# Kernel optimization log

Measured on AMD Instinct MI355X. Metric: run time of the kernel, lower is better.

Reference implementation:

```python
import jax, jax.numpy as jnp
import numpy as np

D = 1024
H = 16
DH = D // H
RATIO = 4
EPS = 1e-5


def layer_norm(x, g, b):
    mu = jnp.mean(x, axis=-1, keepdims=True)
    var = jnp.mean(jnp.square(x - mu), axis=-1, keepdims=True)
    return (x - mu) * jax.lax.rsqrt(var + EPS) * g + b


def setup_inputs() -> dict:
    key = jax.random.key(0)
    ks = jax.random.split(key, 12)
    s = 1.0 / np.sqrt(D)
    inp = {
        "x": jax.random.normal(ks[0], (4, 2048, D), dtype=jnp.float32),
        "Wq": jax.random.normal(ks[1], (D, D), dtype=jnp.float32) * s,
        "bq": jnp.zeros((D,), jnp.float32),
        "Wk": jax.random.normal(ks[2], (D, D), dtype=jnp.float32) * s,
        "bk": jnp.zeros((D,), jnp.float32),
        "Wv": jax.random.normal(ks[3], (D, D), dtype=jnp.float32) * s,
        "bv": jnp.zeros((D,), jnp.float32),
        "Wfc": jax.random.normal(ks[4], (D, D), dtype=jnp.float32) * s,
        "bfc": jnp.zeros((D,), jnp.float32),
        "ln1_g": jnp.ones((D,), jnp.float32),
        "ln1_b": jnp.zeros((D,), jnp.float32),
        "W1": jax.random.normal(ks[5], (D, D * RATIO), dtype=jnp.float32) * s,
        "b1": jnp.zeros((D * RATIO,), jnp.float32),
        "W2": jax.random.normal(ks[6], (D * RATIO, D), dtype=jnp.float32) * (1.0 / np.sqrt(D * RATIO)),
        "b2": jnp.zeros((D,), jnp.float32),
        "ln2_g": jnp.ones((D,), jnp.float32),
        "ln2_b": jnp.zeros((D,), jnp.float32),
    }
    return inp


def reference(x, Wq, bq, Wk, bk, Wv, bv, Wfc, bfc, ln1_g, ln1_b, W1, b1, W2, b2, ln2_g, ln2_b):
    B, S, _ = x.shape
    # QKV projections -> [B, H, S, DH]
    q = (x @ Wq + bq).reshape(B, S, H, DH).transpose(0, 2, 1, 3)
    k = (x @ Wk + bk).reshape(B, S, H, DH).transpose(0, 2, 1, 3)
    v = (x @ Wv + bv).reshape(B, S, H, DH).transpose(0, 2, 1, 3)
    scores = jnp.einsum("bhqd,bhkd->bhqk", q, k) / np.sqrt(DH)
    w = jax.nn.softmax(scores, axis=-1)
    attn = jnp.einsum("bhqk,bhkd->bhqd", w, v)
    attn = attn.transpose(0, 2, 1, 3).reshape(B, S, D)
    attn_out = attn @ Wfc + bfc  # dropout = identity (droprate=0)
    h = layer_norm(x + attn_out, ln1_g, ln1_b)
    m = jax.nn.relu(h @ W1 + b1)
    m = m @ W2 + b2
    # NOTE: original code applies mlp_norm without residual
    return layer_norm(m, ln2_g, ln2_b)
```

## Files before the change

### kernel.cpp

```cpp
#include <hip/hip_runtime.h>
#include <hip/hip_bf16.h>

#define DEV __device__ __forceinline__

typedef __attribute__((ext_vector_type(8))) short short8;
typedef __attribute__((ext_vector_type(4))) float f32x4;

DEV f32x4 mfma16(short8 a, short8 b, f32x4 c) {
  return __builtin_amdgcn_mfma_f32_16x16x32_bf16(a, b, c, 0, 0, 0);
}

DEV unsigned short f2bf(float f) {
  union { float f; unsigned u; } x; x.f = f;
  unsigned r = x.u + 0x7fffu + ((x.u >> 16) & 1u);
  return (unsigned short)(r >> 16);
}

__global__ __launch_bounds__(256) void cvt_bf16(const float* __restrict__ in,
                                                unsigned short* __restrict__ out,
                                                int n4) {
  int i = blockIdx.x * 256 + threadIdx.x;
  if (i >= n4) return;
  float4 v = ((const float4*)in)[i];
  ushort4 o;
  o.x = f2bf(v.x); o.y = f2bf(v.y); o.z = f2bf(v.z); o.w = f2bf(v.w);
  ((ushort4*)out)[i] = o;
}

__global__ __launch_bounds__(256) void cvtT(const float* __restrict__ W,
                                            unsigned short* __restrict__ Wt,
                                            int K, int N) {
  __shared__ float t[32][33];
  int n0 = blockIdx.x * 32, k0 = blockIdx.y * 32;
  int tx = threadIdx.x, ty = threadIdx.y;
#pragma unroll
  for (int i = 0; i < 4; i++)
    t[ty * 4 + i][tx] = W[(size_t)(k0 + ty * 4 + i) * N + n0 + tx];
  __syncthreads();
#pragma unroll
  for (int i = 0; i < 4; i++)
    Wt[(size_t)(n0 + ty * 4 + i) * K + k0 + tx] = f2bf(t[tx][ty * 4 + i]);
}

enum { M_Q = 0, M_K = 1, M_V = 2, M_RES = 3, M_RELU = 4, M_F32 = 5 };

template <int MODE>
__global__ __launch_bounds__(256, 2)
void gemm_bt(const unsigned short* __restrict__ A,
             const unsigned short* __restrict__ Bt,
             const float* __restrict__ bias,
             const float* __restrict__ res,
             void* __restrict__ outp, int M, int N, int K) {
  __shared__ unsigned short lA[128 * 64];
  __shared__ unsigned short lB[128 * 64];
  const int tid = threadIdx.x;
  const int l = tid & 63, w = tid >> 6;
  const int wr = w >> 1, wc = w & 1;
  const int lr = l & 15, lg = l >> 4;
  const int m0 = blockIdx.x * 128, n0 = blockIdx.y * 128;
  f32x4 acc[4][4] = {};

  for (int k0 = 0; k0 < K; k0 += 64) {
    __syncthreads();
#pragma unroll
    for (int i = 0; i < 4; i++) {
      int off = (i * 256 + tid) * 8;
      int r = off >> 6, c = off & 63;
      __builtin_amdgcn_global_load_lds(
          (const __attribute__((address_space(1))) unsigned int*)(A + (size_t)(m0 + r) * K + k0 + c),
          (__attribute__((address_space(3))) unsigned int*)(lA + off), 16, 0, 0);
    }
#pragma unroll
    for (int i = 0; i < 4; i++) {
      int off = (i * 256 + tid) * 8;
      int r = off >> 6, c = off & 63;
      __builtin_amdgcn_global_load_lds(
          (const __attribute__((address_space(1))) unsigned int*)(Bt + (size_t)(n0 + r) * K + k0 + c),
          (__attribute__((address_space(3))) unsigned int*)(lB + off), 16, 0, 0);
    }
    __syncthreads();
#pragma unroll
    for (int kk = 0; kk < 2; kk++) {
      short8 af[4], bfr[4];
#pragma unroll
      for (int mt = 0; mt < 4; mt++)
        af[mt] = *(const short8*)(lA + (wr * 64 + mt * 16 + lr) * 64 + kk * 32 + lg * 8);
#pragma unroll
      for (int nt = 0; nt < 4; nt++)
        bfr[nt] = *(const short8*)(lB + (wc * 64 + nt * 16 + lr) * 64 + kk * 32 + lg * 8);
#pragma unroll
      for (int mt = 0; mt < 4; mt++)
#pragma unroll
        for (int nt = 0; nt < 4; nt++)
          acc[mt][nt] = mfma16(af[mt], bfr[nt], acc[mt][nt]);
    }
  }

#pragma unroll
  for (int mt = 0; mt < 4; mt++) {
#pragma unroll
    for (int nt = 0; nt < 4; nt++) {
#pragma unroll
      for (int r = 0; r < 4; r++) {
        int row = m0 + wr * 64 + mt * 16 + lg * 4 + r;
        int col = n0 + wc * 64 + nt * 16 + lr;
        float v = acc[mt][nt][r] + bias[col];
        if constexpr (MODE == M_Q || MODE == M_K || MODE == M_V) {
          int b = row >> 11, s = row & 2047;
          int h = col >> 6, dh = col & 63;
          if constexpr (MODE == M_Q) {
            ((unsigned short*)outp)[(((size_t)(b * 16 + h) * 2048 + s) << 6) + dh] = f2bf(v * 0.125f);
          } else if constexpr (MODE == M_K) {
            ((unsigned short*)outp)[(((size_t)(b * 16 + h) * 2048 + s) << 6) + dh] = f2bf(v);
          } else {
            ((unsigned short*)outp)[((size_t)(b * 16 + h) * 64 + dh) * 2048 + s] = f2bf(v);
          }
        } else if constexpr (MODE == M_RES) {
          size_t idx = (size_t)row * N + col;
          ((float*)outp)[idx] = v + res[idx];
        } else if constexpr (MODE == M_RELU) {
          ((unsigned short*)outp)[(size_t)row * N + col] = f2bf(v > 0.f ? v : 0.f);
        } else {
          ((float*)outp)[(size_t)row * N + col] = v;
        }
      }
    }
  }
}

__global__ __launch_bounds__(256, 4)
void flash_attn(const unsigned short* __restrict__ Q,
                const unsigned short* __restrict__ Kb,
                const unsigned short* __restrict__ Vt,
                unsigned short* __restrict__ attnb) {
  const int S = 2048;
  __shared__ unsigned short Qs[64 * 64];
  __shared__ unsigned short Ks[2][64 * 64];
  __shared__ unsigned short Vs[2][64 * 64];
  const int tid = threadIdx.x, l = tid & 63, w = tid >> 6;
  const int lr = l & 15, lg = l >> 4;
  const int bh = blockIdx.y, q0 = blockIdx.x * 64;
  const unsigned short* Qp = Q + (size_t)bh * S * 64;
  const unsigned short* Kp = Kb + (size_t)bh * S * 64;
  const unsigned short* Vp = Vt + (size_t)bh * 64 * S;

  auto stage64 = [&](const unsigned short* gbase, size_t rstride, unsigned short* lds) {
#pragma unroll
    for (int i = 0; i < 2; i++) {
      int off16 = i * 256 + tid;
      int r = off16 >> 3;
      int chs = (off16 & 7) ^ (r & 7);
      __builtin_amdgcn_global_load_lds(
          (const __attribute__((address_space(1))) unsigned int*)(gbase + (size_t)r * rstride + chs * 8),
          (__attribute__((address_space(3))) unsigned int*)(lds + (size_t)off16 * 8), 16, 0, 0);
    }
  };

  stage64(Qp + (size_t)q0 * 64, 64, Qs);
  stage64(Kp, 64, Ks[0]);
  stage64(Vp, S, Vs[0]);
  __syncthreads();

  short8 qf[2];
#pragma unroll
  for (int kk = 0; kk < 2; kk++) {
    int rq = w * 16 + lr;
    qf[kk] = *(const short8*)((char*)Qs + rq * 128 + (((kk * 32 + lg * 8) * 2) ^ ((rq & 7) << 4)));
  }
  unsigned short* Pw = Qs + w * 1024;

  float lpart[4] = {0.f, 0.f, 0.f, 0.f};
  f32x4 oacc[4] = {};

  int cur = 0;
  for (int kv0 = 0; kv0 < S; kv0 += 64) {
    if (kv0 + 64 < S) {
      stage64(Kp + (size_t)(kv0 + 64) * 64, 64, Ks[cur ^ 1]);
      stage64(Vp + (kv0 + 64), S, Vs[cur ^ 1]);
    }
    const unsigned short* Kc = Ks[cur];
    const unsigned short* Vc = Vs[cur];

    f32x4 sa[4] = {};
#pragma unroll
    for (int nt = 0; nt < 4; nt++) {
#pragma unroll
      for (int kk = 0; kk < 2; kk++) {
        int rk = nt * 16 + lr;
        short8 kf = *(const short8*)((const char*)Kc + rk * 128 + (((kk * 32 + lg * 8) * 2) ^ ((rk & 7) << 4)));
        sa[nt] = mfma16(qf[kk], kf, sa[nt]);
      }
    }

#pragma unroll
    for (int nt = 0; nt < 4; nt++)
#pragma unroll
      for (int r = 0; r < 4; r++) {
        float p = exp2f(fmaf(sa[nt][r], 1.44269504f, -11.5415603f));
        lpart[r] += p;
        int rr = lg * 4 + r;
        *(unsigned short*)((char*)Pw + rr * 128 + (((nt * 16 + lr) * 2) ^ ((rr & 7) << 4))) =
            (unsigned short)(__float_as_uint(p) >> 16);
      }

#pragma unroll
    for (int kk = 0; kk < 2; kk++) {
      short8 pf = *(const short8*)((char*)Pw + lr * 128 + (((kk * 32 + lg * 8) * 2) ^ ((lr & 7) << 4)));
#pragma unroll
      for (int nt = 0; nt < 4; nt++) {
        int rv = nt * 16 + lr;
        short8 vf = *(const short8*)((const char*)Vc + rv * 128 + (((kk * 32 + lg * 8) * 2) ^ ((rv & 7) << 4)));
        oacc[nt] = mfma16(pf, vf, oacc[nt]);
      }
    }

    __syncthreads();
    cur ^= 1;
  }

#pragma unroll
  for (int d = 1; d < 16; d <<= 1)
#pragma unroll
    for (int r = 0; r < 4; r++) lpart[r] += __shfl_xor(lpart[r], d, 64);

  const int b = bh >> 4, h = bh & 15;
#pragma unroll
  for (int nt = 0; nt < 4; nt++)
#pragma unroll
    for (int r = 0; r < 4; r++) {
      int s = q0 + w * 16 + lg * 4 + r;
      int col = h * 64 + nt * 16 + lr;
      attnb[(size_t)(b * 2048 + s) * 1024 + col] = f2bf(oacc[nt][r] / lpart[r]);
    }
}

template <int OUTF32>
__global__ __launch_bounds__(256)
void ln_row(const float* __restrict__ in, const float* __restrict__ g,
            const float* __restrict__ b, void* __restrict__ outp) {
  const int row = blockIdx.x, tid = threadIdx.x;
  float4 v = ((const float4*)(in + (size_t)row * 1024))[tid];
  float s = v.x + v.y + v.z + v.w;
  float s2 = v.x * v.x + v.y * v.y + v.z * v.z + v.w * v.w;
#pragma unroll
  for (int d = 1; d < 64; d <<= 1) { s += __shfl_xor(s, d, 64); s2 += __shfl_xor(s2, d, 64); }
  __shared__ float ps[8];
  if ((tid & 63) == 0) { ps[tid >> 6] = s; ps[4 + (tid >> 6)] = s2; }
  __syncthreads();
  s = ps[0] + ps[1] + ps[2] + ps[3];
  s2 = ps[4] + ps[5] + ps[6] + ps[7];
  float mu = s * (1.f / 1024.f);
  float var = s2 * (1.f / 1024.f) - mu * mu;
  float rstd = rsqrtf(var + 1e-5f);
  float4 gv = ((const float4*)g)[tid];
  float4 bv = ((const float4*)b)[tid];
  float o0 = (v.x - mu) * rstd * gv.x + bv.x;
  float o1 = (v.y - mu) * rstd * gv.y + bv.y;
  float o2 = (v.z - mu) * rstd * gv.z + bv.z;
  float o3 = (v.w - mu) * rstd * gv.w + bv.w;
  if constexpr (OUTF32) {
    float4 o; o.x = o0; o.y = o1; o.z = o2; o.w = o3;
    ((float4*)outp)[(size_t)row * 256 + tid] = o;
  } else {
    ushort4 o; o.x = f2bf(o0); o.y = f2bf(o1); o.z = f2bf(o2); o.w = f2bf(o3);
    ((ushort4*)outp)[(size_t)row * 256 + tid] = o;
  }
}

extern "C" void kernel_launch(void* const* d_in, const int* in_sizes, int n_in,
                              void* d_out, int out_size, void* d_ws, size_t ws_size,
                              hipStream_t stream) {
  const float* x   = (const float*)d_in[0];
  const float* Wq  = (const float*)d_in[1];
  const float* bq  = (const float*)d_in[2];
  const float* Wk  = (const float*)d_in[3];
  const float* bk  = (const float*)d_in[4];
  const float* Wv  = (const float*)d_in[5];
  const float* bv  = (const float*)d_in[6];
  const float* Wfc = (const float*)d_in[7];
  const float* bfc = (const float*)d_in[8];
  const float* g1  = (const float*)d_in[9];
  const float* bn1 = (const float*)d_in[10];
  const float* W1  = (const float*)d_in[11];
  const float* b1  = (const float*)d_in[12];
  const float* W2  = (const float*)d_in[13];
  const float* b2  = (const float*)d_in[14];
  const float* g2  = (const float*)d_in[15];
  const float* bn2 = (const float*)d_in[16];

  char* ws = (char*)d_ws;
  size_t off = 0;
  auto alloc = [&](size_t bytes) { size_t o = off; off += (bytes + 255) & ~(size_t)255; return o; };
  unsigned short* xb  = (unsigned short*)(ws + alloc(8192UL * 1024 * 2));
  unsigned short* Wqt = (unsigned short*)(ws + alloc(1024UL * 1024 * 2));
  unsigned short* Wkt = (unsigned short*)(ws + alloc(1024UL * 1024 * 2));
  unsigned short* Wvt = (unsigned short*)(ws + alloc(1024UL * 1024 * 2));
  unsigned short* Wft = (unsigned short*)(ws + alloc(1024UL * 1024 * 2));
  unsigned short* W1t = (unsigned short*)(ws + alloc(4096UL * 1024 * 2));
  unsigned short* W2t = (unsigned short*)(ws + alloc(1024UL * 4096 * 2));
  char* zoneA = ws + alloc(67108864UL);
  float* y    = (float*)(ws + alloc(33554432UL));
  unsigned short* hb = (unsigned short*)(ws + alloc(16777216UL));

  unsigned short* Qb    = (unsigned short*)zoneA;
  unsigned short* Kbuf  = Qb + 8388608;
  unsigned short* Vtb   = Kbuf + 8388608;
  unsigned short* attnb = Vtb + 8388608;
  unsigned short* mb    = (unsigned short*)zoneA;
  float* m2 = y;

  dim3 tb(32, 8);
  cvt_bf16<<<8192, 256, 0, stream>>>(x, xb, 2097152);
  cvtT<<<dim3(32, 32), tb, 0, stream>>>(Wq, Wqt, 1024, 1024);
  cvtT<<<dim3(32, 32), tb, 0, stream>>>(Wk, Wkt, 1024, 1024);
  cvtT<<<dim3(32, 32), tb, 0, stream>>>(Wv, Wvt, 1024, 1024);
  cvtT<<<dim3(32, 32), tb, 0, stream>>>(Wfc, Wft, 1024, 1024);
  cvtT<<<dim3(128, 32), tb, 0, stream>>>(W1, W1t, 1024, 4096);
  cvtT<<<dim3(32, 128), tb, 0, stream>>>(W2, W2t, 4096, 1024);

  gemm_bt<M_Q><<<dim3(64, 8), 256, 0, stream>>>(xb, Wqt, bq, nullptr, Qb, 8192, 1024, 1024);
  gemm_bt<M_K><<<dim3(64, 8), 256, 0, stream>>>(xb, Wkt, bk, nullptr, Kbuf, 8192, 1024, 1024);
  gemm_bt<M_V><<<dim3(64, 8), 256, 0, stream>>>(xb, Wvt, bv, nullptr, Vtb, 8192, 1024, 1024);

  flash_attn<<<dim3(32, 64), 256, 0, stream>>>(Qb, Kbuf, Vtb, attnb);

  gemm_bt<M_RES><<<dim3(64, 8), 256, 0, stream>>>(attnb, Wft, bfc, x, y, 8192, 1024, 1024);
  ln_row<0><<<8192, 256, 0, stream>>>(y, g1, bn1, hb);
  gemm_bt<M_RELU><<<dim3(64, 32), 256, 0, stream>>>(hb, W1t, b1, nullptr, mb, 8192, 4096, 1024);
  gemm_bt<M_F32><<<dim3(64, 8), 256, 0, stream>>>(mb, W2t, b2, nullptr, m2, 8192, 1024, 4096);
  ln_row<1><<<8192, 256, 0, stream>>>(m2, g2, bn2, d_out);
}
```

Baseline: 601.1 us.

## Fuse QKV GEMMs, add XCD-aware block swizzle, precompute flash-attn LDS addresses

The three Q/K/V projection GEMMs become one launch with N=3072. Each 1024-column section picks its own bias, scale and output layout (V stays transposed). This relies on the transposed Wq/Wk/Wv buffers being contiguous in the workspace. Both the GEMM and attention kernels remap block indices so consecutive blocks on the same XCD share A/B or K/V tiles in L2. The flash-attention inner loop also hoists the swizzled LDS offsets out of the loop to cut per-iteration integer address work.

```diff
diff --git a/kernel.cpp b/kernel.cpp
--- a/kernel.cpp
+++ b/kernel.cpp
@@ -42,13 +42,15 @@
     Wt[(size_t)(n0 + ty * 4 + i) * K + k0 + tx] = f2bf(t[tx][ty * 4 + i]);
 }
 
-enum { M_Q = 0, M_K = 1, M_V = 2, M_RES = 3, M_RELU = 4, M_F32 = 5 };
+enum { M_QKV = 0, M_RES = 3, M_RELU = 4, M_F32 = 5 };
 
 template <int MODE>
 __global__ __launch_bounds__(256, 2)
 void gemm_bt(const unsigned short* __restrict__ A,
              const unsigned short* __restrict__ Bt,
              const float* __restrict__ bias,
+             const float* __restrict__ bias2,
+             const float* __restrict__ bias3,
              const float* __restrict__ res,
              void* __restrict__ outp, int M, int N, int K) {
   __shared__ unsigned short lA[128 * 64];
@@ -57,7 +59,10 @@
   const int l = tid & 63, w = tid >> 6;
   const int wr = w >> 1, wc = w & 1;
   const int lr = l & 15, lg = l >> 4;
-  const int m0 = blockIdx.x * 128, n0 = blockIdx.y * 128;
+  const int lin = blockIdx.y * gridDim.x + blockIdx.x;
+  const int cpx = (gridDim.x * gridDim.y) >> 3;
+  const int swz = (lin & 7) * cpx + (lin >> 3);
+  const int m0 = (swz % gridDim.x) * 128, n0 = (swz / gridDim.x) * 128;
   f32x4 acc[4][4] = {};
 
   for (int k0 = 0; k0 < K; k0 += 64) {
@@ -96,6 +101,10 @@
     }
   }
 
+  const int sect = n0 >> 10;
+  const float* bp = bias;
+  if constexpr (MODE == M_QKV) bp = sect == 0 ? bias : (sect == 1 ? bias2 : bias3);
+
 #pragma unroll
   for (int mt = 0; mt < 4; mt++) {
 #pragma unroll
@@ -104,24 +113,28 @@
       for (int r = 0; r < 4; r++) {
         int row = m0 + wr * 64 + mt * 16 + lg * 4 + r;
         int col = n0 + wc * 64 + nt * 16 + lr;
-        float v = acc[mt][nt][r] + bias[col];
-        if constexpr (MODE == M_Q || MODE == M_K || MODE == M_V) {
+        if constexpr (MODE == M_QKV) {
+          int c10 = col & 1023;
+          float v = acc[mt][nt][r] + bp[c10];
           int b = row >> 11, s = row & 2047;
-          int h = col >> 6, dh = col & 63;
-          if constexpr (MODE == M_Q) {
-            ((unsigned short*)outp)[(((size_t)(b * 16 + h) * 2048 + s) << 6) + dh] = f2bf(v * 0.125f);
-          } else if constexpr (MODE == M_K) {
-            ((unsigned short*)outp)[(((size_t)(b * 16 + h) * 2048 + s) << 6) + dh] = f2bf(v);
+          int h = c10 >> 6, dh = c10 & 63;
+          unsigned short* o = (unsigned short*)outp;
+          if (sect == 2) {
+            o[(size_t)2 * 8388608 + ((size_t)(b * 16 + h) * 64 + dh) * 2048 + s] = f2bf(v);
           } else {
-            ((unsigned short*)outp)[((size_t)(b * 16 + h) * 64 + dh) * 2048 + s] = f2bf(v);
+            float sc = sect == 0 ? 0.125f : 1.f;
+            o[(size_t)sect * 8388608 + (((size_t)(b * 16 + h) * 2048 + s) << 6) + dh] = f2bf(v * sc);
           }
-        } else if constexpr (MODE == M_RES) {
-          size_t idx = (size_t)row * N + col;
-          ((float*)outp)[idx] = v + res[idx];
-        } else if constexpr (MODE == M_RELU) {
-          ((unsigned short*)outp)[(size_t)row * N + col] = f2bf(v > 0.f ? v : 0.f);
         } else {
-          ((float*)outp)[(size_t)row * N + col] = v;
+          float v = acc[mt][nt][r] + bias[col];
+          if constexpr (MODE == M_RES) {
+            size_t idx = (size_t)row * N + col;
+            ((float*)outp)[idx] = v + res[idx];
+          } else if constexpr (MODE == M_RELU) {
+            ((unsigned short*)outp)[(size_t)row * N + col] = f2bf(v > 0.f ? v : 0.f);
+          } else {
+            ((float*)outp)[(size_t)row * N + col] = v;
+          }
         }
       }
     }
@@ -139,7 +152,9 @@
   __shared__ unsigned short Vs[2][64 * 64];
   const int tid = threadIdx.x, l = tid & 63, w = tid >> 6;
   const int lr = l & 15, lg = l >> 4;
-  const int bh = blockIdx.y, q0 = blockIdx.x * 64;
+  const int lin = blockIdx.y * gridDim.x + blockIdx.x;
+  const int sw = (lin & 7) * 256 + (lin >> 3);
+  const int q0 = (sw & 31) * 64, bh = sw >> 5;
   const unsigned short* Qp = Q + (size_t)bh * S * 64;
   const unsigned short* Kp = Kb + (size_t)bh * S * 64;
   const unsigned short* Vp = Vt + (size_t)bh * 64 * S;
@@ -161,13 +176,20 @@
   stage64(Vp, S, Vs[0]);
   __syncthreads();
 
+  const int swzl = (lr & 7) << 4;
+  const int kcol0 = (lg * 16) ^ swzl;
+  const int kcol1 = (64 + lg * 16) ^ swzl;
+  const int lr128 = lr * 128;
+
   short8 qf[2];
-#pragma unroll
-  for (int kk = 0; kk < 2; kk++) {
-    int rq = w * 16 + lr;
-    qf[kk] = *(const short8*)((char*)Qs + rq * 128 + (((kk * 32 + lg * 8) * 2) ^ ((rq & 7) << 4)));
+  {
+    const char* Qb_ = (const char*)Qs + (w * 16 + lr) * 128;
+    qf[0] = *(const short8*)(Qb_ + kcol0);
+    qf[1] = *(const short8*)(Qb_ + kcol1);
   }
   unsigned short* Pw = Qs + w * 1024;
+  char* Pwb = (char*)Pw;
+  const int pcol = lr * 2;
 
   float lpart[4] = {0.f, 0.f, 0.f, 0.f};
   f32x4 oacc[4] = {};
@@ -178,40 +200,42 @@
       stage64(Kp + (size_t)(kv0 + 64) * 64, 64, Ks[cur ^ 1]);
       stage64(Vp + (kv0 + 64), S, Vs[cur ^ 1]);
     }
-    const unsigned short* Kc = Ks[cur];
-    const unsigned short* Vc = Vs[cur];
+    const char* Kc0 = (const char*)Ks[cur] + lr128 + kcol0;
+    const char* Kc1 = (const char*)Ks[cur] + lr128 + kcol1;
+    const char* Vc0 = (const char*)Vs[cur] + lr128 + kcol0;
+    const char* Vc1 = (const char*)Vs[cur] + lr128 + kcol1;
 
     f32x4 sa[4] = {};
 #pragma unroll
     for (int nt = 0; nt < 4; nt++) {
-#pragma unroll
-      for (int kk = 0; kk < 2; kk++) {
-        int rk = nt * 16 + lr;
-        short8 kf = *(const short8*)((const char*)Kc + rk * 128 + (((kk * 32 + lg * 8) * 2) ^ ((rk & 7) << 4)));
-        sa[nt] = mfma16(qf[kk], kf, sa[nt]);
-      }
-    }
-
-#pragma unroll
-    for (int nt = 0; nt < 4; nt++)
-#pragma unroll
-      for (int r = 0; r < 4; r++) {
+      sa[nt] = mfma16(qf[0], *(const short8*)(Kc0 + nt * 2048), sa[nt]);
+      sa[nt] = mfma16(qf[1], *(const short8*)(Kc1 + nt * 2048), sa[nt]);
+    }
+
+#pragma unroll
+    for (int r = 0; r < 4; r++) {
+      int rr = lg * 4 + r;
+      char* baser = Pwb + rr * 128;
+      int swzr = (rr & 7) << 4;
+#pragma unroll
+      for (int nt = 0; nt < 4; nt++) {
         float p = exp2f(fmaf(sa[nt][r], 1.44269504f, -11.5415603f));
         lpart[r] += p;
-        int rr = lg * 4 + r;
-        *(unsigned short*)((char*)Pw + rr * 128 + (((nt * 16 + lr) * 2) ^ ((rr & 7) << 4))) =
+        *(unsigned short*)(baser + ((nt * 32 + pcol) ^ swzr)) =
             (unsigned short)(__float_as_uint(p) >> 16);
       }
-
-#pragma unroll
-    for (int kk = 0; kk < 2; kk++) {
-      short8 pf = *(const short8*)((char*)Pw + lr * 128 + (((kk * 32 + lg * 8) * 2) ^ ((lr & 7) << 4)));
-#pragma unroll
-      for (int nt = 0; nt < 4; nt++) {
-        int rv = nt * 16 + lr;
-        short8 vf = *(const short8*)((const char*)Vc + rv * 128 + (((kk * 32 + lg * 8) * 2) ^ ((rv & 7) << 4)));
-        oacc[nt] = mfma16(pf, vf, oacc[nt]);
-      }
+    }
+
+    short8 pf0, pf1;
+    {
+      const char* Pb_ = Pwb + lr128;
+      pf0 = *(const short8*)(Pb_ + kcol0);
+      pf1 = *(const short8*)(Pb_ + kcol1);
+    }
+#pragma unroll
+    for (int nt = 0; nt < 4; nt++) {
+      oacc[nt] = mfma16(pf0, *(const short8*)(Vc0 + nt * 2048), oacc[nt]);
+      oacc[nt] = mfma16(pf1, *(const short8*)(Vc1 + nt * 2048), oacc[nt]);
     }
 
     __syncthreads();
@@ -318,15 +342,13 @@
   cvtT<<<dim3(128, 32), tb, 0, stream>>>(W1, W1t, 1024, 4096);
   cvtT<<<dim3(32, 128), tb, 0, stream>>>(W2, W2t, 4096, 1024);
 
-  gemm_bt<M_Q><<<dim3(64, 8), 256, 0, stream>>>(xb, Wqt, bq, nullptr, Qb, 8192, 1024, 1024);
-  gemm_bt<M_K><<<dim3(64, 8), 256, 0, stream>>>(xb, Wkt, bk, nullptr, Kbuf, 8192, 1024, 1024);
-  gemm_bt<M_V><<<dim3(64, 8), 256, 0, stream>>>(xb, Wvt, bv, nullptr, Vtb, 8192, 1024, 1024);
+  gemm_bt<M_QKV><<<dim3(64, 24), 256, 0, stream>>>(xb, Wqt, bq, bk, bv, nullptr, Qb, 8192, 3072, 1024);
 
   flash_attn<<<dim3(32, 64), 256, 0, stream>>>(Qb, Kbuf, Vtb, attnb);
 
-  gemm_bt<M_RES><<<dim3(64, 8), 256, 0, stream>>>(attnb, Wft, bfc, x, y, 8192, 1024, 1024);
+  gemm_bt<M_RES><<<dim3(64, 8), 256, 0, stream>>>(attnb, Wft, bfc, nullptr, nullptr, x, y, 8192, 1024, 1024);
   ln_row<0><<<8192, 256, 0, stream>>>(y, g1, bn1, hb);
-  gemm_bt<M_RELU><<<dim3(64, 32), 256, 0, stream>>>(hb, W1t, b1, nullptr, mb, 8192, 4096, 1024);
-  gemm_bt<M_F32><<<dim3(64, 8), 256, 0, stream>>>(mb, W2t, b2, nullptr, m2, 8192, 1024, 4096);
+  gemm_bt<M_RELU><<<dim3(64, 32), 256, 0, stream>>>(hb, W1t, b1, nullptr, nullptr, nullptr, mb, 8192, 4096, 1024);
+  gemm_bt<M_F32><<<dim3(64, 8), 256, 0, stream>>>(mb, W2t, b2, nullptr, nullptr, nullptr, m2, 8192, 1024, 4096);
   ln_row<1><<<8192, 256, 0, stream>>>(m2, g2, bn2, d_out);
 }
```

Result: slower. 626.2 us (+4.2%).
